# Optimization experiments

Hardware: AMD Instinct MI355X
Metric: run time of the kernel (lower is better)

The kernel has to match this reference:

```python
import jax, jax.numpy as jnp
import numpy as np

B, V, M, H, T = 512, 256, 128, 512, 16  # batch, vocab, memory_size, hidden_dim, timing_dim
ALPHA = 0.95


def setup_inputs() -> dict:
    key = jax.random.key(0)
    ks = jax.random.split(key, 8)
    return {
        "x": jax.random.uniform(ks[0], (B, V), dtype=jnp.float32),
        "memory": jax.random.normal(ks[1], (B, M, V), dtype=jnp.float32),
        "memory_timings": jax.random.randint(ks[2], (B, M), 0, 1000, dtype=jnp.int64) if jax.config.jax_enable_x64 else jax.random.randint(ks[2], (B, M), 0, 1000).astype(jnp.int32),
        "memory_surprise": jax.random.uniform(ks[3], (B, M), dtype=jnp.float32),
        "last_prediction": jax.random.uniform(ks[4], (B, V), dtype=jnp.float32),
        "W1": jax.random.normal(ks[5], (V * M + M * T, H), dtype=jnp.float32) * 0.01,
        "b1": jnp.zeros((H,), dtype=jnp.float32),
        "W2": jax.random.normal(ks[6], (H, V), dtype=jnp.float32) * 0.01,
        "b2": jnp.zeros((V,), dtype=jnp.float32),
    }


def reference(x, memory, memory_timings, memory_surprise, last_prediction, W1, b1, W2, b2):
    b = x.shape[0]
    ar = jnp.arange(b)
    # compute_surprise
    surprise = -jnp.sum(x * jnp.log(last_prediction + 1e-6), axis=1)  # [B]
    # update_memory_timings
    timings = memory_timings + 1
    msurp = memory_surprise * ALPHA
    # update_memory: argmin-scatter into memory/timings/surprise
    idx = jnp.argmin(msurp, axis=1)  # [B]
    memory = memory.at[ar, idx].set(x)
    timings = timings.at[ar, idx].set(0)
    msurp = msurp.at[ar, idx].set(surprise)
    # compute_prediction: sort by timing, gather-reorder memory
    order = jnp.argsort(timings, axis=1)  # stable ascending, [B, M]
    sorted_t = jnp.take_along_axis(timings, order, axis=1)  # [B, M]
    sorted_mem = jnp.take_along_axis(memory, order[:, :, None], axis=1)  # [B, M, V]
    # binary encoding of timings: (t // 2**k) % 2 for k in [0, T)
    bits = ((sorted_t[:, :, None] >> jnp.arange(T)) & 1).astype(jnp.float32)  # [B, M, T]
    pred_in = jnp.concatenate([sorted_mem.reshape(b, -1), bits.reshape(b, -1)], axis=1)
    h = jax.nn.relu(pred_in @ W1 + b1)
    return h @ W2 + b2
```

## Files before the change

kernel.cpp:

```cpp
#include <hip/hip_runtime.h>

typedef unsigned int uint;
typedef unsigned short ushort;
typedef __attribute__((ext_vector_type(8))) short short8;
typedef __attribute__((ext_vector_type(4))) float f32x4;

#define B_   512
#define V_   256
#define M_   128
#define H_   512
#define T_   16
#define KTOT 34816

__device__ __forceinline__ ushort f2bf(float f) {
  uint u = __builtin_bit_cast(uint, f);
  u += 0x7fffu + ((u >> 16) & 1u);
  return (ushort)(u >> 16);
}
__device__ __forceinline__ float bf2f(ushort s) {
  return __builtin_bit_cast(float, ((uint)s) << 16);
}

__device__ __forceinline__ int swz_k(int k, int row) {
  return (k & ~31) | (((((k >> 3) & 3) ^ ((row >> 1) & 3)) << 3)) | (k & 7);
}

__global__ __launch_bounds__(256) void prep_kernel(
    const float* __restrict__ x, const float* __restrict__ mem,
    const int* __restrict__ timings, const float* __restrict__ msurp,
    const float* __restrict__ b1,
    ushort* __restrict__ A, float* __restrict__ h_pre)
{
  const int b = blockIdx.x, tid = threadIdx.x;
  __shared__ int s_t[M_];
  __shared__ int s_row[M_];
  __shared__ int s_st[M_];
  __shared__ int s_idx;

  if (tid < 64) {
    float v0 = msurp[b * M_ + tid];
    float v1 = msurp[b * M_ + tid + 64];
    float v; int i;
    if (v1 < v0) { v = v1; i = tid + 64; } else { v = v0; i = tid; }
    #pragma unroll
    for (int off = 32; off > 0; off >>= 1) {
      float ov = __shfl_down(v, off);
      int   oi = __shfl_down(i, off);
      if (ov < v || (ov == v && oi < i)) { v = ov; i = oi; }
    }
    if (tid == 0) s_idx = i;
  }
  __syncthreads();
  const int idx = s_idx;

  if (tid < M_) {
    int t = timings[b * M_ + tid] + 1;
    if (tid == idx) t = 0;
    s_t[tid] = t;
  }
  h_pre[(size_t)b * H_ + tid]       = b1[tid];
  h_pre[(size_t)b * H_ + 256 + tid] = b1[256 + tid];
  __syncthreads();

  if (tid < M_) {
    const int t = s_t[tid];
    int r = 0;
    for (int j = 0; j < M_; ++j) {
      int tj = s_t[j];
      r += (tj < t || (tj == t && j < tid)) ? 1 : 0;
    }
    s_row[r] = tid;
    s_st[r]  = t;
  }
  __syncthreads();

  if (tid < M_) {
    const int t = s_st[tid];
    uint p[8];
    #pragma unroll
    for (int h = 0; h < 8; ++h) {
      uint lo = ((t >> (2 * h)) & 1) ? 0x3F80u : 0u;
      uint hi = ((t >> (2 * h + 1)) & 1) ? 0x3F80u : 0u;
      p[h] = lo | (hi << 16);
    }
    const int k0 = V_ * M_ + tid * T_;
    uint4 w0; w0.x = p[0]; w0.y = p[1]; w0.z = p[2]; w0.w = p[3];
    uint4 w1; w1.x = p[4]; w1.y = p[5]; w1.z = p[6]; w1.w = p[7];
    *(uint4*)(A + (size_t)b * KTOT + swz_k(k0, b))     = w0;
    *(uint4*)(A + (size_t)b * KTOT + swz_k(k0 + 8, b)) = w1;
  }

  const int lane = tid & 63, sub = tid >> 6;
  for (int it = 0; it < 32; ++it) {
    const int slot = it * 4 + sub;
    const int rowm = s_row[slot];
    const float* src = (rowm == idx) ? (x + (size_t)b * V_)
                                     : (mem + ((size_t)b * M_ + rowm) * V_);
    f32x4 v = *(const f32x4*)(src + lane * 4);
    uint2 o;
    o.x = (uint)f2bf(v[0]) | ((uint)f2bf(v[1]) << 16);
    o.y = (uint)f2bf(v[2]) | ((uint)f2bf(v[3]) << 16);
    const int k = slot * V_ + lane * 4;
    *(uint2*)(A + (size_t)b * KTOT + swz_k(k, b)) = o;
  }
}

#define BM 256
#define BN 256
#define SPLITK 64
#define KCH 544
#define NCHU 17

#define GLD16(g, l) __builtin_amdgcn_global_load_lds( \
  (const __attribute__((address_space(1))) void*)(g), \
  (__attribute__((address_space(3))) void*)(l), 16, 0, 0)

template<bool USE_ATOMIC>
__global__ __launch_bounds__(512, 2) void gemm1_kernel(
    const ushort* __restrict__ A, const float* __restrict__ W1,
    void* __restrict__ dstv)
{
  __shared__ __align__(16) ushort As[3][BM * 32];
  __shared__ __align__(16) ushort Bs[2][BN * 32];

  const int bid  = blockIdx.x;
  const int sk   = (bid & 7) | ((bid >> 5) << 3);
  const int tile = (bid >> 3) & 3;
  const int b0   = (tile >> 1) * BM;
  const int n0   = (tile & 1) * BN;
  const int tid  = threadIdx.x, wave = tid >> 6, lane = tid & 63;
  const int wm   = wave >> 1;
  const int wn   = wave & 1;
  const long kb0 = (long)sk * KCH;

  f32x4 acc[4][8];
  #pragma unroll
  for (int i = 0; i < 4; ++i)
    #pragma unroll
    for (int j = 0; j < 8; ++j) acc[i][j] = (f32x4)0.f;

  const int ar  = wave * 32 + (lane >> 2);
  const int akk = (lane & 3) * 8;
  auto stageA = [&](int buf, int chunk) {
    const long kb = kb0 + (long)chunk * 32;
    GLD16(A + ((size_t)(b0 + ar))      * KTOT + kb + akk, &As[buf][(wave * 32) * 32]);
    GLD16(A + ((size_t)(b0 + ar + 16)) * KTOT + kb + akk, &As[buf][(wave * 32 + 16) * 32]);
  };

  const int ncol = tid & 255;
  const int kh   = tid >> 8;
  const float* w1p = W1 + (size_t)(kb0 + kh * 16) * H_ + n0 + ncol;
  const int sg   = (ncol >> 1) & 3;
  const int kc0  = kh * 2;
  const int bw0  = ncol * 32 + ((kc0 ^ sg) * 8);
  const int bw1  = ncol * 32 + (((kc0 + 1) ^ sg) * 8);

  auto loadB = [&](float* r, int c) {
    const float* p = w1p + (size_t)c * 32 * H_;
    #pragma unroll
    for (int i = 0; i < 16; ++i) r[i] = p[(size_t)i * H_];
  };
  auto writeB = [&](const float* r, ushort* base) {
    uint4 o0, o1;
    o0.x = (uint)f2bf(r[0])  | ((uint)f2bf(r[1])  << 16);
    o0.y = (uint)f2bf(r[2])  | ((uint)f2bf(r[3])  << 16);
    o0.z = (uint)f2bf(r[4])  | ((uint)f2bf(r[5])  << 16);
    o0.w = (uint)f2bf(r[6])  | ((uint)f2bf(r[7])  << 16);
    o1.x = (uint)f2bf(r[8])  | ((uint)f2bf(r[9])  << 16);
    o1.y = (uint)f2bf(r[10]) | ((uint)f2bf(r[11]) << 16);
    o1.z = (uint)f2bf(r[12]) | ((uint)f2bf(r[13]) << 16);
    o1.w = (uint)f2bf(r[14]) | ((uint)f2bf(r[15]) << 16);
    *(uint4*)(base + bw0) = o0;
    *(uint4*)(base + bw1) = o1;
  };

  const int xo     = (((lane >> 4) ^ ((lane >> 1) & 3)) * 8);
  const int a_roff = (wm * 64 + (lane & 15)) * 32;
  const int b_roff = (wn * 128 + (lane & 15)) * 32;

  float brE[16], brO[16];

#define GITER(c, BRL, BRW, ISSUE, WRITE, VMC) do {                            \
    asm volatile("s_waitcnt vmcnt(" VMC ") lgkmcnt(0)" ::: "memory");         \
    __builtin_amdgcn_s_barrier();                                             \
    __builtin_amdgcn_sched_barrier(0);                                        \
    if (ISSUE) { stageA(((c) + 2) % 3, (c) + 2); loadB(BRL, (c) + 2); }       \
    const ushort* as_ = &As[(c) % 3][a_roff + xo];                            \
    const ushort* bs_ = &Bs[(c) & 1][b_roff + xo];                            \
    short8 af[4], bf[4];                                                      \
    _Pragma("unroll") for (int i = 0; i < 4; ++i)                             \
      af[i] = *(const short8*)(as_ + i * 16 * 32);                            \
    _Pragma("unroll") for (int j = 0; j < 4; ++j)                             \
      bf[j] = *(const short8*)(bs_ + j * 16 * 32);                            \
    _Pragma("unroll") for (int i = 0; i < 4; ++i)                             \
      _Pragma("unroll") for (int j = 0; j < 4; ++j)                           \
        acc[i][j] = __builtin_amdgcn_mfma_f32_16x16x32_bf16(af[i], bf[j],     \
                                                            acc[i][j], 0,0,0);\
    _Pragma("unroll") for (int j = 0; j < 4; ++j)                             \
      bf[j] = *(const short8*)(bs_ + (j + 4) * 16 * 32);                      \
    _Pragma("unroll") for (int i = 0; i < 4; ++i)                             \
      _Pragma("unroll") for (int j = 0; j < 4; ++j)                           \
        acc[i][j + 4] = __builtin_amdgcn_mfma_f32_16x16x32_bf16(af[i], bf[j], \
                                                            acc[i][j + 4],    \
                                                            0, 0, 0);         \
    if (WRITE) writeB(BRW, &Bs[((c) + 1) & 1][0]);                            \
  } while (0)

  stageA(0, 0);
  loadB(brE, 0);
  stageA(1, 1);
  loadB(brO, 1);
  writeB(brE, &Bs[0][0]);

  #pragma unroll 1
  for (int cc = 0; cc < 14; cc += 2) {
    GITER(cc,     brE, brO, true, true, "18");
    GITER(cc + 1, brO, brE, true, true, "18");
  }
  GITER(14, brE, brO, true,  true,  "18");
  GITER(15, brO, brE, false, true,  "18");
  GITER(16, brE, brO, false, false, "0");
#undef GITER

  const int row0 = b0 + wm * 64 + (lane >> 4) * 4;
  const int col0 = n0 + wn * 128 + (lane & 15);
  if constexpr (USE_ATOMIC) {
    float* dst = (float*)dstv;
    #pragma unroll
    for (int i = 0; i < 4; ++i)
      #pragma unroll
      for (int j = 0; j < 8; ++j)
        #pragma unroll
        for (int r = 0; r < 4; ++r)
          atomicAdd(&dst[(size_t)(row0 + i * 16 + r) * H_ + col0 + j * 16], acc[i][j][r]);
  } else {
    ushort* P = (ushort*)dstv + (size_t)sk * (B_ * H_);
    #pragma unroll
    for (int i = 0; i < 4; ++i)
      #pragma unroll
      for (int j = 0; j < 8; ++j)
        #pragma unroll
        for (int r = 0; r < 4; ++r)
          P[(size_t)(row0 + i * 16 + r) * H_ + col0 + j * 16] = f2bf(acc[i][j][r]);
  }
}

template<bool FROM_PARTIALS>
__global__ __launch_bounds__(256) void gemm2_kernel(
    const void* __restrict__ Pin, const float* __restrict__ b1,
    const float* __restrict__ W2, const float* __restrict__ b2,
    float* __restrict__ out)
{
  const int bb = blockIdx.x * 2;
  const int v  = threadIdx.x;
  __shared__ float hs[2][H_];

  {
    const int id  = v * 4;
    const int row = id >> 9, col = id & 511;
    f32x4 s;
    if constexpr (FROM_PARTIALS) {
      const ushort* P = (const ushort*)Pin;
      s = *(const f32x4*)(b1 + col);
      #pragma unroll 4
      for (int sk = 0; sk < SPLITK; ++sk) {
        uint2 u = *(const uint2*)(P + (size_t)sk * (B_ * H_) + (size_t)(bb + row) * H_ + col);
        s[0] += bf2f((ushort)(u.x & 0xffff));
        s[1] += bf2f((ushort)(u.x >> 16));
        s[2] += bf2f((ushort)(u.y & 0xffff));
        s[3] += bf2f((ushort)(u.y >> 16));
      }
    } else {
      s = *(const f32x4*)((const float*)Pin + (size_t)(bb + row) * H_ + col);
    }
    f32x4 r;
    #pragma unroll
    for (int t = 0; t < 4; ++t) r[t] = fmaxf(s[t], 0.f);
    *(f32x4*)&hs[row][col] = r;
  }
  __syncthreads();

  float a0 = 0.f, a1 = 0.f;
  for (int j4 = 0; j4 < H_ / 4; ++j4) {
    f32x4 h0 = *(const f32x4*)&hs[0][j4 * 4];
    f32x4 h1 = *(const f32x4*)&hs[1][j4 * 4];
    #pragma unroll
    for (int t = 0; t < 4; ++t) {
      float w = W2[(size_t)(j4 * 4 + t) * V_ + v];
      a0 += h0[t] * w; a1 += h1[t] * w;
    }
  }
  const float bias = b2[v];
  out[(size_t)(bb + 0) * V_ + v] = a0 + bias;
  out[(size_t)(bb + 1) * V_ + v] = a1 + bias;
}

extern "C" void kernel_launch(void* const* d_in, const int* in_sizes, int n_in,
                              void* d_out, int out_size, void* d_ws, size_t ws_size,
                              hipStream_t stream) {
  const float* x   = (const float*)d_in[0];
  const float* mem = (const float*)d_in[1];
  const int*   tim = (const int*)d_in[2];
  const float* msu = (const float*)d_in[3];
  const float* W1  = (const float*)d_in[5];
  const float* b1  = (const float*)d_in[6];
  const float* W2  = (const float*)d_in[7];
  const float* b2  = (const float*)d_in[8];
  float* out = (float*)d_out;

  char* ws = (char*)d_ws;
  const size_t abytes = (size_t)B_ * KTOT * 2;
  const size_t pbytes = (size_t)SPLITK * B_ * H_ * 2;
  const size_t hbytes = (size_t)B_ * H_ * 4;
  const bool partials = ws_size >= abytes + pbytes + hbytes;

  ushort* A_ws  = (ushort*)ws;
  void*   P     = (void*)(ws + abytes);
  float*  h_pre = partials ? (float*)(ws + abytes + pbytes)
                           : (float*)(ws + abytes);

  prep_kernel<<<B_, 256, 0, stream>>>(x, mem, tim, msu, b1, A_ws, h_pre);
  if (partials) {
    gemm1_kernel<false><<<4 * SPLITK, 512, 0, stream>>>(A_ws, W1, P);
    gemm2_kernel<true><<<B_ / 2, 256, 0, stream>>>(P, b1, W2, b2, out);
  } else {
    gemm1_kernel<true><<<4 * SPLITK, 512, 0, stream>>>(A_ws, W1, h_pre);
    gemm2_kernel<false><<<B_ / 2, 256, 0, stream>>>(h_pre, b1, W2, b2, out);
  }
}
```

Baseline: 75.02 us.

## Reshape GEMM1 block tile to full-batch 512x128 to cut W1 reads

Changes the GEMM1 block tile from 256x256 to 512x128, so each block covers the whole batch and a quarter of the hidden columns. Each wave now owns 64 rows and all 128 columns. The point is that every fp32 W1 element is loaded and converted to bf16 only once across the batch, halving W1 global traffic, which dominates this kernel. In exchange, A tiles are staged twice as often (four async loads per wave per chunk), the per-thread B register buffers shrink to 8 values, and the vmcnt wait thresholds are retuned to match.

Result: no change. 75.19 us (+0.2%).

```diff
diff --git a/kernel.cpp b/kernel.cpp
--- a/kernel.cpp
+++ b/kernel.cpp
@@ -105,8 +105,8 @@
   }
 }
 
-#define BM 256
-#define BN 256
+#define BM 512
+#define BN 128
 #define SPLITK 64
 #define KCH 544
 #define NCHU 17
@@ -126,11 +126,8 @@
   const int bid  = blockIdx.x;
   const int sk   = (bid & 7) | ((bid >> 5) << 3);
   const int tile = (bid >> 3) & 3;
-  const int b0   = (tile >> 1) * BM;
-  const int n0   = (tile & 1) * BN;
+  const int n0   = tile * BN;
   const int tid  = threadIdx.x, wave = tid >> 6, lane = tid & 63;
-  const int wm   = wave >> 1;
-  const int wn   = wave & 1;
   const long kb0 = (long)sk * KCH;
 
   f32x4 acc[4][8];
@@ -139,46 +136,40 @@
     #pragma unroll
     for (int j = 0; j < 8; ++j) acc[i][j] = (f32x4)0.f;
 
-  const int ar  = wave * 32 + (lane >> 2);
+  const int ar  = wave * 64 + (lane >> 2);
   const int akk = (lane & 3) * 8;
   auto stageA = [&](int buf, int chunk) {
     const long kb = kb0 + (long)chunk * 32;
-    GLD16(A + ((size_t)(b0 + ar))      * KTOT + kb + akk, &As[buf][(wave * 32) * 32]);
-    GLD16(A + ((size_t)(b0 + ar + 16)) * KTOT + kb + akk, &As[buf][(wave * 32 + 16) * 32]);
+    #pragma unroll
+    for (int q = 0; q < 4; ++q)
+      GLD16(A + ((size_t)(ar + q * 16)) * KTOT + kb + akk,
+            &As[buf][(wave * 64 + q * 16) * 32]);
   };
 
-  const int ncol = tid & 255;
-  const int kh   = tid >> 8;
-  const float* w1p = W1 + (size_t)(kb0 + kh * 16) * H_ + n0 + ncol;
-  const int sg   = (ncol >> 1) & 3;
-  const int kc0  = kh * 2;
-  const int bw0  = ncol * 32 + ((kc0 ^ sg) * 8);
-  const int bw1  = ncol * 32 + (((kc0 + 1) ^ sg) * 8);
+  const int ncol = tid & 127;
+  const int koct = tid >> 7;
+  const float* w1p = W1 + (size_t)(kb0 + koct * 8) * H_ + n0 + ncol;
+  const int b_woff = ncol * 32 + ((koct ^ ((ncol >> 1) & 3)) * 8);
 
   auto loadB = [&](float* r, int c) {
     const float* p = w1p + (size_t)c * 32 * H_;
     #pragma unroll
-    for (int i = 0; i < 16; ++i) r[i] = p[(size_t)i * H_];
+    for (int i = 0; i < 8; ++i) r[i] = p[(size_t)i * H_];
   };
   auto writeB = [&](const float* r, ushort* base) {
-    uint4 o0, o1;
-    o0.x = (uint)f2bf(r[0])  | ((uint)f2bf(r[1])  << 16);
-    o0.y = (uint)f2bf(r[2])  | ((uint)f2bf(r[3])  << 16);
-    o0.z = (uint)f2bf(r[4])  | ((uint)f2bf(r[5])  << 16);
-    o0.w = (uint)f2bf(r[6])  | ((uint)f2bf(r[7])  << 16);
-    o1.x = (uint)f2bf(r[8])  | ((uint)f2bf(r[9])  << 16);
-    o1.y = (uint)f2bf(r[10]) | ((uint)f2bf(r[11]) << 16);
-    o1.z = (uint)f2bf(r[12]) | ((uint)f2bf(r[13]) << 16);
-    o1.w = (uint)f2bf(r[14]) | ((uint)f2bf(r[15]) << 16);
-    *(uint4*)(base + bw0) = o0;
-    *(uint4*)(base + bw1) = o1;
+    uint4 o;
+    o.x = (uint)f2bf(r[0]) | ((uint)f2bf(r[1]) << 16);
+    o.y = (uint)f2bf(r[2]) | ((uint)f2bf(r[3]) << 16);
+    o.z = (uint)f2bf(r[4]) | ((uint)f2bf(r[5]) << 16);
+    o.w = (uint)f2bf(r[6]) | ((uint)f2bf(r[7]) << 16);
+    *(uint4*)(base + b_woff) = o;
   };
 
   const int xo     = (((lane >> 4) ^ ((lane >> 1) & 3)) * 8);
-  const int a_roff = (wm * 64 + (lane & 15)) * 32;
-  const int b_roff = (wn * 128 + (lane & 15)) * 32;
-
-  float brE[16], brO[16];
+  const int a_roff = (wave * 64 + (lane & 15)) * 32;
+  const int b_roff = (lane & 15) * 32;
+
+  float brE[8], brO[8];
 
 #define GITER(c, BRL, BRW, ISSUE, WRITE, VMC) do {                            \
     asm volatile("s_waitcnt vmcnt(" VMC ") lgkmcnt(0)" ::: "memory");         \
@@ -214,16 +205,16 @@
 
   #pragma unroll 1
   for (int cc = 0; cc < 14; cc += 2) {
-    GITER(cc,     brE, brO, true, true, "18");
-    GITER(cc + 1, brO, brE, true, true, "18");
-  }
-  GITER(14, brE, brO, true,  true,  "18");
-  GITER(15, brO, brE, false, true,  "18");
+    GITER(cc,     brE, brO, true, true, "12");
+    GITER(cc + 1, brO, brE, true, true, "12");
+  }
+  GITER(14, brE, brO, true,  true,  "12");
+  GITER(15, brO, brE, false, true,  "12");
   GITER(16, brE, brO, false, false, "0");
 #undef GITER
 
-  const int row0 = b0 + wm * 64 + (lane >> 4) * 4;
-  const int col0 = n0 + wn * 128 + (lane & 15);
+  const int row0 = wave * 64 + (lane >> 4) * 4;
+  const int col0 = n0 + (lane & 15);
   if constexpr (USE_ATOMIC) {
     float* dst = (float*)dstv;
     #pragma unroll
```
